# Optimization experiments

Measured on AMD Instinct MI355X. Metric: run time of the kernel, lower is better.

## Reference

```python
import jax, jax.numpy as jnp
import numpy as np

B, CIN, H, W = 2, 3, 768, 768
CB = 32          # backbone out_channels (= channels_mid for heads)
ORDER = 5
MARGIN = 3.0     # ScaledTanh margin of refinement head


def _conv(x, w, b, pad):
    # x: [N,C,H,W], w: [O,I,kh,kw]
    y = jax.lax.conv_general_dilated(x, w, (1, 1), [(pad, pad), (pad, pad)],
                                     dimension_numbers=('NCHW', 'OIHW', 'NCHW'))
    return y + b[None, :, None, None]


def _readout(x, w1, b1, s, t, w2, b2, pad):
    # conv(k) -> batchnorm(eval, folded to scale/shift) -> relu -> dropout(eval=id) -> conv1x1
    h = _conv(x, w1, b1, pad)
    h = jax.nn.relu(h * s[None, :, None, None] + t[None, :, None, None])
    return _conv(h, w2, b2, 0)


def setup_inputs() -> dict:
    key = jax.random.key(0)
    ks = iter(jax.random.split(key, 16))
    def rn(shape, scale=0.05):
        return jax.random.normal(next(ks), shape, jnp.float32) * scale
    d = {'inputs': jax.random.normal(next(ks), (B, CIN, H, W), jnp.float32)}
    d['bb_w'] = rn((CB, CIN, 3, 3)); d['bb_b'] = jnp.zeros((CB,), jnp.float32)
    def head(name, k, cout):
        d[name + '_w1'] = rn((CB, CB, k, k)); d[name + '_b1'] = jnp.zeros((CB,), jnp.float32)
        d[name + '_s'] = jnp.ones((CB,), jnp.float32); d[name + '_t'] = jnp.zeros((CB,), jnp.float32)
        d[name + '_w2'] = rn((cout, CB, 1, 1)); d[name + '_b2'] = jnp.zeros((cout,), jnp.float32)
    head('score', 3, 2)
    head('loc', 7, 2)
    head('four', 7, ORDER * 4)
    head('ref', 7, 2)
    return d


def reference(inputs, bb_w, bb_b,
              score_w1, score_b1, score_s, score_t, score_w2, score_b2,
              loc_w1, loc_b1, loc_s, loc_t, loc_w2, loc_b2,
              four_w1, four_b1, four_s, four_t, four_w2, four_b2,
              ref_w1, ref_b1, ref_s, ref_t, ref_w2, ref_b2):
    # backbone (simple conv + relu; out_channels is an int so contour == refinement features)
    feats = jax.nn.relu(_conv(inputs, bb_w, bb_b, 1))
    scores = _readout(feats, score_w1, score_b1, score_s, score_t, score_w2, score_b2, 1)
    locations = _readout(feats, loc_w1, loc_b1, loc_s, loc_t, loc_w2, loc_b2, 3)
    fourier = _readout(feats, four_w1, four_b1, four_s, four_t, four_w2, four_b2, 3)
    # ReadOut final activation ScaledTanh(3.0), then CPNCore multiplies by internal margin 1.0;
    # feature HW == input HW (stride 1), so F.interpolate is a no-op.
    refinement = jnp.tanh(_readout(feats, ref_w1, ref_b1, ref_s, ref_t, ref_w2, ref_b2, 3)) * MARGIN
    return (scores, locations, refinement, fourier)
```

## Files before the change

kernel.cpp:

```cpp
#include <hip/hip_runtime.h>
#include <hip/hip_bf16.h>
#include <cmath>

#define HH 768
#define WW 768
#define HWSZ (768*768)

typedef __attribute__((ext_vector_type(8))) short bhalf8;
typedef __attribute__((ext_vector_type(4))) float f32x4;
typedef __attribute__((ext_vector_type(16))) float f32x16;

__device__ inline ushort f2bf(float f) {
  __hip_bfloat16 h = __float2bfloat16(f);
  return *reinterpret_cast<ushort*>(&h);
}
__device__ inline float bf2f(ushort u) {
  union { unsigned int i; float f; } v; v.i = ((unsigned int)u) << 16; return v.f;
}

__global__ __launch_bounds__(256) void wxform_all_kernel(
    const float* __restrict__ w1S, const float* __restrict__ b1S,
    const float* __restrict__ sS,  const float* __restrict__ tS,
    const float* __restrict__ w1L, const float* __restrict__ b1L,
    const float* __restrict__ sL,  const float* __restrict__ tL,
    const float* __restrict__ w1F, const float* __restrict__ b1F,
    const float* __restrict__ sF,  const float* __restrict__ tF,
    const float* __restrict__ w1R, const float* __restrict__ b1R,
    const float* __restrict__ sR,  const float* __restrict__ tR,
    ushort* __restrict__ wT0, float* __restrict__ bb0, size_t wt_stride_elems)
{
  int h = blockIdx.y;
  const float *w1, *b1, *s, *t;
  int npos;
  if (h == 0)      { w1 = w1S; b1 = b1S; s = sS; t = tS; npos = 9;  }
  else if (h == 1) { w1 = w1L; b1 = b1L; s = sL; t = tL; npos = 49; }
  else if (h == 2) { w1 = w1F; b1 = b1F; s = sF; t = tF; npos = 49; }
  else             { w1 = w1R; b1 = b1R; s = sR; t = tR; npos = 49; }

  ushort* wT = wT0 + (size_t)h * wt_stride_elems;
  float*  bb = bb0 + h * 32;

  int i = blockIdx.x * 256 + threadIdx.x;
  if (i < npos * 1024) {
    int pos = i >> 10, mc = i & 1023, m = mc >> 5, c = mc & 31;
    wT[i] = f2bf(w1[(m * 32 + c) * npos + pos] * s[m]);
  }
  if (blockIdx.x == 0 && i < 32) bb[i] = b1[i] * s[i] + t[i];
}

__global__ __launch_bounds__(256) void backbone_kernel(
    const float* __restrict__ x, const float* __restrict__ w,
    const float* __restrict__ bias, ushort* __restrict__ feats)
{
  int p = blockIdx.x * 256 + threadIdx.x;
  int bb  = p / HWSZ;
  int rem = p - bb * HWSZ;
  int y   = rem / WW;
  int xx  = rem - y * WW;
  const float* xb = x + (size_t)bb * 3 * HWSZ;

  float v[3][3][3];
  #pragma unroll
  for (int c = 0; c < 3; c++)
    #pragma unroll
    for (int dy = 0; dy < 3; dy++)
      #pragma unroll
      for (int dx = 0; dx < 3; dx++) {
        int yy = y + dy - 1, xq = xx + dx - 1;
        v[c][dy][dx] = (yy >= 0 && yy < HH && xq >= 0 && xq < WW)
                         ? xb[(size_t)c * HWSZ + yy * WW + xq] : 0.f;
      }

  union { ushort u[32]; uint4 q[4]; } pk;
  #pragma unroll
  for (int o = 0; o < 32; o++) {
    float acc = bias[o];
    #pragma unroll
    for (int c = 0; c < 3; c++)
      #pragma unroll
      for (int dy = 0; dy < 3; dy++)
        #pragma unroll
        for (int dx = 0; dx < 3; dx++)
          acc = fmaf(w[((o * 3 + c) * 3 + dy) * 3 + dx], v[c][dy][dx], acc);
    pk.u[o] = f2bf(fmaxf(acc, 0.f));
  }
  uint4* dst = (uint4*)(feats + ((size_t)bb * HWSZ + rem) * 32);
  #pragma unroll
  for (int i = 0; i < 4; i++) dst[i] = pk.q[i];
}

template <int COUT, bool DO_TANH>
__device__ inline void head_epilogue3(
    const f32x16 acc[2], const float* __restrict__ bbh,
    const float* __restrict__ w2, const float* __restrict__ b2,
    float* __restrict__ out_base, ushort* mid,
    int wv, int qr, int qc, int kg, int by, int bx, int bb)
{
  #pragma unroll
  for (int n = 0; n < 2; n++) {
    int px = (2 * wv + qr) * 32 + n * 16 + qc;
    #pragma unroll
    for (int rg = 0; rg < 4; rg++) {
      int m0 = 8 * rg + 4 * kg;
      ushort u[4];
      #pragma unroll
      for (int j = 0; j < 4; j++)
        u[j] = f2bf(fmaxf(acc[n][rg * 4 + j] + bbh[m0 + j], 0.f));
      uint2 pkv;
      pkv.x = (unsigned int)u[0] | ((unsigned int)u[1] << 16);
      pkv.y = (unsigned int)u[2] | ((unsigned int)u[3] << 16);
      *(uint2*)(mid + px * 36 + m0) = pkv;
    }
  }
  __syncthreads();

  int t = threadIdx.x;
  float mv[32];
  #pragma unroll
  for (int j = 0; j < 8; j++) {
    uint2 r = *(const uint2*)(mid + t * 36 + j * 4);
    mv[j * 4 + 0] = bf2f((ushort)(r.x & 0xffff));
    mv[j * 4 + 1] = bf2f((ushort)(r.x >> 16));
    mv[j * 4 + 2] = bf2f((ushort)(r.y & 0xffff));
    mv[j * 4 + 3] = bf2f((ushort)(r.y >> 16));
  }
  int oy = by * 16 + (t >> 5), ox = bx * 32 + (t & 31);
  size_t opix = (size_t)oy * WW + ox;
  float* ob = out_base + (size_t)bb * COUT * HWSZ;
  #pragma unroll
  for (int oc = 0; oc < COUT; oc++) {
    float a2 = b2[oc];
    #pragma unroll
    for (int m = 0; m < 32; m++) a2 = fmaf(w2[oc * 32 + m], mv[m], a2);
    if (DO_TANH) a2 = tanhf(a2) * 3.0f;
    ob[(size_t)oc * HWSZ + opix] = a2;
  }
  __syncthreads();
}

__global__ __launch_bounds__(512, 4) void heads3_kernel(
    const ushort* __restrict__ feats,
    const ushort* __restrict__ wtL, const ushort* __restrict__ wtF,
    const ushort* __restrict__ wtR,
    const float* __restrict__ bbL, const float* __restrict__ bbF,
    const float* __restrict__ bbR,
    const float* __restrict__ w2L, const float* __restrict__ b2L,
    const float* __restrict__ w2F, const float* __restrict__ b2F,
    const float* __restrict__ w2R, const float* __restrict__ b2R,
    float* __restrict__ outL, float* __restrict__ outF, float* __restrict__ outR)
{
  __shared__ __align__(16) char smem[53504 + 24576];
  ushort* tile = (ushort*)smem;
  ushort* wrow = (ushort*)(smem + 53504);

  int bx = blockIdx.x % 24;
  int by = (blockIdx.x / 24) % 48;
  int bb = blockIdx.x / 1152;
  int x0 = bx * 32 - 3, y0 = by * 16 - 3;
  const ushort* fB = feats + (size_t)bb * HWSZ * 32;

  for (int p = threadIdx.x; p < 22 * 38; p += 512) {
    int r = p / 38, cl = p - r * 38;
    int yy = y0 + r, xx = x0 + cl;
    uint4 q0 = {0,0,0,0}, q1 = {0,0,0,0}, q2 = {0,0,0,0}, q3 = {0,0,0,0};
    if (yy >= 0 && yy < HH && xx >= 0 && xx < WW) {
      const uint4* src = (const uint4*)(fB + ((size_t)yy * WW + xx) * 32);
      q0 = src[0]; q1 = src[1]; q2 = src[2]; q3 = src[3];
    }
    ushort* dst = tile + r * 1216 + cl * 8;
    *(uint4*)(dst +   0) = q0;
    *(uint4*)(dst + 304) = q1;
    *(uint4*)(dst + 608) = q2;
    *(uint4*)(dst + 912) = q3;
  }

  int tid = threadIdx.x;
  int l  = tid & 63;
  int wv = tid >> 6;
  int q  = l & 31;
  int kg = l >> 5;
  int qr = q >> 4, qc = q & 15;

  const ushort* pb  = tile + (2 * wv + qr) * 1216 + kg * 304 + qc * 8;
  const ushort* aB  = wrow + kg * 256 + q * 8;
  const ushort* aGL = wtL + q * 32 + kg * 8;
  const ushort* aGF = wtF + q * 32 + kg * 8;
  const ushort* aGR = wtR + q * 32 + kg * 8;

  int st_kx[3], st_src_off[3];
  const ushort* st_base[3];
  #pragma unroll
  for (int j = 0; j < 3; j++) {
    int idx = j * 512 + tid;
    int kx = idx >> 8, rem = idx & 255;
    int h = rem >> 7, g = (rem >> 5) & 3, m = rem & 31;
    st_kx[j] = idx;
    st_base[j] = h ? wtF : wtL;
    st_src_off[j] = kx * 1024 + m * 32 + g * 8;
  }

  f32x16 accL[2] = {};
  f32x16 accF[2] = {};
  f32x16 accR[2] = {};

  #pragma unroll 1
  for (int ky = 0; ky < 7; ky++) {
    __syncthreads();
    #pragma unroll
    for (int j = 0; j < 3; j++) {
      bhalf8 v = *(const bhalf8*)(st_base[j] + ky * 7168 + st_src_off[j]);
      *(bhalf8*)(wrow + st_kx[j] * 8) = v;
    }
    __syncthreads();

    const ushort* pbrow = pb + ky * 1216;
    const ushort* aR = aGR + ky * 7168;

    #pragma unroll
    for (int kx = 0; kx < 7; kx++) {
      bhalf8 fL[2], fF[2], fR[2];
      #pragma unroll
      for (int kh = 0; kh < 2; kh++) {
        if (kx < 6) {
          fL[kh] = *(const bhalf8*)(aB + kx * 2048 +        kh * 512);
          fF[kh] = *(const bhalf8*)(aB + kx * 2048 + 1024 + kh * 512);
        } else {
          fL[kh] = *(const bhalf8*)(aGL + ky * 7168 + 6144 + kh * 16);
          fF[kh] = *(const bhalf8*)(aGF + ky * 7168 + 6144 + kh * 16);
        }
        fR[kh] = *(const bhalf8*)(aR + kx * 1024 + kh * 16);
      }
      bhalf8 bfr[2][2];
      #pragma unroll
      for (int n = 0; n < 2; n++)
        #pragma unroll
        for (int kh = 0; kh < 2; kh++)
          bfr[n][kh] = *(const bhalf8*)(pbrow + kh * 608 + n * 128 + kx * 8);

      #pragma unroll
      for (int n = 0; n < 2; n++)
        #pragma unroll
        for (int kh = 0; kh < 2; kh++) {
          accL[n] = __builtin_amdgcn_mfma_f32_32x32x16_bf16(fL[kh], bfr[n][kh], accL[n], 0, 0, 0);
          accF[n] = __builtin_amdgcn_mfma_f32_32x32x16_bf16(fF[kh], bfr[n][kh], accF[n], 0, 0, 0);
          accR[n] = __builtin_amdgcn_mfma_f32_32x32x16_bf16(fR[kh], bfr[n][kh], accR[n], 0, 0, 0);
        }
    }
  }

  __syncthreads();
  ushort* mid = (ushort*)smem;

  head_epilogue3<2,  false>(accL, bbL, w2L, b2L, outL, mid, wv, qr, qc, kg, by, bx, bb);
  head_epilogue3<20, false>(accF, bbF, w2F, b2F, outF, mid, wv, qr, qc, kg, by, bx, bb);
  head_epilogue3<2,  true >(accR, bbR, w2R, b2R, outR, mid, wv, qr, qc, kg, by, bx, bb);
}

typedef __attribute__((ext_vector_type(4))) float f32x4b;
template <int COUT, bool DO_TANH>
__device__ inline void head_epilogue_s(
    const f32x16 acc[2], const float* __restrict__ bbh,
    const float* __restrict__ w2, const float* __restrict__ b2,
    float* __restrict__ out_base, float* mid,
    int wv, int qr, int qc, int kg, int by, int bx, int bb)
{
  #pragma unroll
  for (int n = 0; n < 2; n++) {
    int pix = (wv * 4 + 2 * n + qr) * 16 + qc;
    #pragma unroll
    for (int rg = 0; rg < 4; rg++) {
      int m0 = 8 * rg + 4 * kg;
      f32x4 v;
      #pragma unroll
      for (int j = 0; j < 4; j++)
        v[j] = fmaxf(acc[n][rg * 4 + j] + bbh[m0 + j], 0.f);
      *(f32x4*)(mid + pix * 36 + m0) = v;
    }
  }
  __syncthreads();

  int t = threadIdx.x;
  float mv[32];
  #pragma unroll
  for (int j2 = 0; j2 < 8; j2++)
    *(f32x4*)(mv + 4 * j2) = *(const f32x4*)(mid + t * 36 + 4 * j2);

  int oy = by * 16 + (t >> 4), ox = bx * 16 + (t & 15);
  size_t opix = (size_t)oy * WW + ox;
  float* ob = out_base + (size_t)bb * COUT * HWSZ;
  #pragma unroll
  for (int oc = 0; oc < COUT; oc++) {
    float a2 = b2[oc];
    #pragma unroll
    for (int m = 0; m < 32; m++) a2 = fmaf(w2[oc * 32 + m], mv[m], a2);
    if (DO_TANH) a2 = tanhf(a2) * 3.0f;
    ob[(size_t)oc * HWSZ + opix] = a2;
  }
}

__global__ __launch_bounds__(256, 4) void score_kernel(
    const ushort* __restrict__ feats,
    const ushort* __restrict__ wtS, const float* __restrict__ bbS,
    const float* __restrict__ w2S, const float* __restrict__ b2S,
    float* __restrict__ outS)
{
  constexpr int TW = 18, CPAD = 40;
  constexpr int SMEM_BYTES = 256 * 36 * 4;
  __shared__ __align__(16) char smem[SMEM_BYTES];
  ushort* tile = (ushort*)smem;

  int bx = blockIdx.x % 48;
  int by = (blockIdx.x / 48) % 48;
  int bb = blockIdx.x / 2304;
  int x0 = bx * 16 - 1, y0 = by * 16 - 1;
  const ushort* fB = feats + (size_t)bb * HWSZ * 32;

  for (int p = threadIdx.x; p < TW * TW; p += 256) {
    int py = p / TW, pxx = p % TW;
    int yy = y0 + py, xx = x0 + pxx;
    uint4 q0 = {0,0,0,0}, q1 = {0,0,0,0}, q2 = {0,0,0,0}, q3 = {0,0,0,0};
    if (yy >= 0 && yy < HH && xx >= 0 && xx < WW) {
      const uint4* src = (const uint4*)(fB + ((size_t)yy * WW + xx) * 32);
      q0 = src[0]; q1 = src[1]; q2 = src[2]; q3 = src[3];
    }
    uint4* dst = (uint4*)(tile + (size_t)p * CPAD);
    dst[0] = q0; dst[1] = q1; dst[2] = q2; dst[3] = q3;
  }
  __syncthreads();

  int l  = threadIdx.x & 63;
  int wv = threadIdx.x >> 6;
  int q  = l & 31;
  int kg = l >> 5;
  int qr = q >> 4, qc = q & 15;

  const ushort* pb = tile + ((wv * 4 + qr) * TW + qc) * CPAD + kg * 8;
  const int aoff = q * 32 + kg * 8;

  f32x16 acc[2] = {};

  #pragma unroll
  for (int ky = 0; ky < 3; ky++) {
    #pragma unroll
    for (int kx = 0; kx < 3; kx++) {
      const int tap = ky * 3 + kx;
      bhalf8 a0[2];
      #pragma unroll
      for (int kh = 0; kh < 2; kh++)
        a0[kh] = *(const bhalf8*)(wtS + tap * 1024 + aoff + kh * 16);
      #pragma unroll
      for (int n = 0; n < 2; n++) {
        #pragma unroll
        for (int kh = 0; kh < 2; kh++) {
          bhalf8 bf = *(const bhalf8*)(pb + (ky * TW + kx) * CPAD
                                          + n * 2 * TW * CPAD + kh * 16);
          acc[n] = __builtin_amdgcn_mfma_f32_32x32x16_bf16(a0[kh], bf, acc[n], 0, 0, 0);
        }
      }
    }
  }

  __syncthreads();
  float* mid = (float*)smem;
  head_epilogue_s<2, false>(acc, bbS, w2S, b2S, outS, mid, wv, qr, qc, kg, by, bx, bb);
}

extern "C" void kernel_launch(void* const* d_in, const int* in_sizes, int n_in,
                              void* d_out, int out_size, void* d_ws, size_t ws_size,
                              hipStream_t stream) {
  const float* input = (const float*)d_in[0];
  const float* bb_w  = (const float*)d_in[1];
  const float* bb_b  = (const float*)d_in[2];

  ushort* feats = (ushort*)d_ws;
  char* base = (char*)d_ws;
  const size_t FEATS_BYTES = (size_t)2 * HWSZ * 32 * 2;
  const size_t WT_STRIDE_E = 49 * 1024;
  ushort* wT0 = (ushort*)(base + FEATS_BYTES);
  float*  bb0 = (float*)(base + FEATS_BYTES + 4 * WT_STRIDE_E * 2);
  (void)out_size; (void)ws_size; (void)n_in; (void)in_sizes;

  float* out = (float*)d_out;
  float* outS = out;
  float* outL = out + (size_t)4  * HWSZ;
  float* outR = out + (size_t)8  * HWSZ;
  float* outF = out + (size_t)12 * HWSZ;

  dim3 wxgrid(196, 4);
  wxform_all_kernel<<<wxgrid, 256, 0, stream>>>(
      (const float*)d_in[3],  (const float*)d_in[4],  (const float*)d_in[5],  (const float*)d_in[6],
      (const float*)d_in[9],  (const float*)d_in[10], (const float*)d_in[11], (const float*)d_in[12],
      (const float*)d_in[15], (const float*)d_in[16], (const float*)d_in[17], (const float*)d_in[18],
      (const float*)d_in[21], (const float*)d_in[22], (const float*)d_in[23], (const float*)d_in[24],
      wT0, bb0, WT_STRIDE_E);

  backbone_kernel<<<4608, 256, 0, stream>>>(input, bb_w, bb_b, feats);

  const ushort* wtS = wT0 + 0 * WT_STRIDE_E;
  const ushort* wtL = wT0 + 1 * WT_STRIDE_E;
  const ushort* wtF = wT0 + 2 * WT_STRIDE_E;
  const ushort* wtR = wT0 + 3 * WT_STRIDE_E;

  heads3_kernel<<<2 * 48 * 24, 512, 0, stream>>>(
      feats, wtL, wtF, wtR,
      bb0 + 32, bb0 + 64, bb0 + 96,
      (const float*)d_in[13], (const float*)d_in[14],
      (const float*)d_in[19], (const float*)d_in[20],
      (const float*)d_in[25], (const float*)d_in[26],
      outL, outF, outR);

  score_kernel<<<2 * 48 * 48, 256, 0, stream>>>(
      feats, wtS, bb0 + 0,
      (const float*)d_in[7], (const float*)d_in[8], outS);
}
```

Baseline: 435.1 us.

## Prefetch next weight row into registers and raise MFMA wave priority

```diff
diff --git a/kernel.cpp b/kernel.cpp
--- a/kernel.cpp
+++ b/kernel.cpp
@@ -138,7 +138,7 @@
   __syncthreads();
 }
 
-__global__ __launch_bounds__(512, 4) void heads3_kernel(
+__global__ __launch_bounds__(512, 2) void heads3_kernel(
     const ushort* __restrict__ feats,
     const ushort* __restrict__ wtL, const ushort* __restrict__ wtF,
     const ushort* __restrict__ wtR,
@@ -187,17 +187,24 @@
   const ushort* aGF = wtF + q * 32 + kg * 8;
   const ushort* aGR = wtR + q * 32 + kg * 8;
 
-  int st_kx[3], st_src_off[3];
-  const ushort* st_base[3];
-  #pragma unroll
-  for (int j = 0; j < 3; j++) {
-    int idx = j * 512 + tid;
-    int kx = idx >> 8, rem = idx & 255;
-    int h = rem >> 7, g = (rem >> 5) & 3, m = rem & 31;
-    st_kx[j] = idx;
-    st_base[j] = h ? wtF : wtL;
-    st_src_off[j] = kx * 1024 + m * 32 + g * 8;
-  }
+  const ushort* stp0; const ushort* stp1; const ushort* stp2;
+  {
+    int idx, kx, rem, h, g, m;
+    idx = tid;        kx = idx >> 8; rem = idx & 255; h = rem >> 7; g = (rem >> 5) & 3; m = rem & 31;
+    stp0 = (h ? wtF : wtL) + kx * 1024 + m * 32 + g * 8;
+    idx = 512 + tid;  kx = idx >> 8; rem = idx & 255; h = rem >> 7; g = (rem >> 5) & 3; m = rem & 31;
+    stp1 = (h ? wtF : wtL) + kx * 1024 + m * 32 + g * 8;
+    idx = 1024 + tid; kx = idx >> 8; rem = idx & 255; h = rem >> 7; g = (rem >> 5) & 3; m = rem & 31;
+    stp2 = (h ? wtF : wtL) + kx * 1024 + m * 32 + g * 8;
+  }
+  ushort* std0 = wrow + (size_t)tid * 8;
+  ushort* std1 = wrow + (size_t)(512 + tid) * 8;
+  ushort* std2 = wrow + (size_t)(1024 + tid) * 8;
+
+  bhalf8 pA0 = *(const bhalf8*)(stp0);
+  bhalf8 pA1 = *(const bhalf8*)(stp1);
+  bhalf8 pA2 = *(const bhalf8*)(stp2);
+  bhalf8 pB0 = pA0, pB1 = pA1, pB2 = pA2;
 
   f32x16 accL[2] = {};
   f32x16 accF[2] = {};
@@ -206,12 +213,16 @@
   #pragma unroll 1
   for (int ky = 0; ky < 7; ky++) {
     __syncthreads();
-    #pragma unroll
-    for (int j = 0; j < 3; j++) {
-      bhalf8 v = *(const bhalf8*)(st_base[j] + ky * 7168 + st_src_off[j]);
-      *(bhalf8*)(wrow + st_kx[j] * 8) = v;
-    }
+    *(bhalf8*)std0 = pA0;
+    *(bhalf8*)std1 = pA1;
+    *(bhalf8*)std2 = pA2;
     __syncthreads();
+
+    if (ky < 6) {
+      pB0 = *(const bhalf8*)(stp0 + (ky + 1) * 7168);
+      pB1 = *(const bhalf8*)(stp1 + (ky + 1) * 7168);
+      pB2 = *(const bhalf8*)(stp2 + (ky + 1) * 7168);
+    }
 
     const ushort* pbrow = pb + ky * 1216;
     const ushort* aR = aGR + ky * 7168;
@@ -237,6 +248,7 @@
         for (int kh = 0; kh < 2; kh++)
           bfr[n][kh] = *(const bhalf8*)(pbrow + kh * 608 + n * 128 + kx * 8);
 
+      __builtin_amdgcn_s_setprio(1);
       #pragma unroll
       for (int n = 0; n < 2; n++)
         #pragma unroll
@@ -245,7 +257,10 @@
           accF[n] = __builtin_amdgcn_mfma_f32_32x32x16_bf16(fF[kh], bfr[n][kh], accF[n], 0, 0, 0);
           accR[n] = __builtin_amdgcn_mfma_f32_32x32x16_bf16(fR[kh], bfr[n][kh], accR[n], 0, 0, 0);
         }
-    }
+      __builtin_amdgcn_s_setprio(0);
+    }
+
+    pA0 = pB0; pA1 = pB1; pA2 = pB2;
   }
 
   __syncthreads();
@@ -256,7 +271,6 @@
   head_epilogue3<2,  true >(accR, bbR, w2R, b2R, outR, mid, wv, qr, qc, kg, by, bx, bb);
 }
 
-typedef __attribute__((ext_vector_type(4))) float f32x4b;
 template <int COUT, bool DO_TANH>
 __device__ inline void head_epilogue_s(
     const f32x16 acc[2], const float* __restrict__ bbh,
```

Measured after the change: 427.9 us. About the same (-1.6%).

## Load head weights directly from global with register prefetch, drop LDS weight staging

Applied to the files above, without the earlier changes.

```diff
diff --git a/kernel.cpp b/kernel.cpp
--- a/kernel.cpp
+++ b/kernel.cpp
@@ -138,7 +138,7 @@
   __syncthreads();
 }
 
-__global__ __launch_bounds__(512, 4) void heads3_kernel(
+__global__ __launch_bounds__(512, 2) void heads3_kernel(
     const ushort* __restrict__ feats,
     const ushort* __restrict__ wtL, const ushort* __restrict__ wtF,
     const ushort* __restrict__ wtR,
@@ -149,9 +149,8 @@
     const float* __restrict__ w2R, const float* __restrict__ b2R,
     float* __restrict__ outL, float* __restrict__ outF, float* __restrict__ outR)
 {
-  __shared__ __align__(16) char smem[53504 + 24576];
+  __shared__ __align__(16) char smem[53504];
   ushort* tile = (ushort*)smem;
-  ushort* wrow = (ushort*)(smem + 53504);
 
   int bx = blockIdx.x % 24;
   int by = (blockIdx.x / 24) % 48;
@@ -173,6 +172,7 @@
     *(uint4*)(dst + 608) = q2;
     *(uint4*)(dst + 912) = q3;
   }
+  __syncthreads();
 
   int tid = threadIdx.x;
   int l  = tid & 63;
@@ -182,69 +182,77 @@
   int qr = q >> 4, qc = q & 15;
 
   const ushort* pb  = tile + (2 * wv + qr) * 1216 + kg * 304 + qc * 8;
-  const ushort* aB  = wrow + kg * 256 + q * 8;
   const ushort* aGL = wtL + q * 32 + kg * 8;
   const ushort* aGF = wtF + q * 32 + kg * 8;
   const ushort* aGR = wtR + q * 32 + kg * 8;
 
-  int st_kx[3], st_src_off[3];
-  const ushort* st_base[3];
-  #pragma unroll
-  for (int j = 0; j < 3; j++) {
-    int idx = j * 512 + tid;
-    int kx = idx >> 8, rem = idx & 255;
-    int h = rem >> 7, g = (rem >> 5) & 3, m = rem & 31;
-    st_kx[j] = idx;
-    st_base[j] = h ? wtF : wtL;
-    st_src_off[j] = kx * 1024 + m * 32 + g * 8;
-  }
-
   f32x16 accL[2] = {};
   f32x16 accF[2] = {};
   f32x16 accR[2] = {};
 
   #pragma unroll 1
   for (int ky = 0; ky < 7; ky++) {
-    __syncthreads();
-    #pragma unroll
-    for (int j = 0; j < 3; j++) {
-      bhalf8 v = *(const bhalf8*)(st_base[j] + ky * 7168 + st_src_off[j]);
-      *(bhalf8*)(wrow + st_kx[j] * 8) = v;
-    }
-    __syncthreads();
-
+    const ushort* aL = aGL + ky * 7168;
+    const ushort* aF = aGF + ky * 7168;
+    const ushort* aR = aGR + ky * 7168;
     const ushort* pbrow = pb + ky * 1216;
-    const ushort* aR = aGR + ky * 7168;
+
+    bhalf8 fL[7][2], fF[7][2], fR[7][2];
+    #pragma unroll
+    for (int kx = 0; kx < 2; kx++) {
+      fL[kx][0] = *(const bhalf8*)(aL + kx * 1024);
+      fL[kx][1] = *(const bhalf8*)(aL + kx * 1024 + 16);
+      fF[kx][0] = *(const bhalf8*)(aF + kx * 1024);
+      fF[kx][1] = *(const bhalf8*)(aF + kx * 1024 + 16);
+      fR[kx][0] = *(const bhalf8*)(aR + kx * 1024);
+      fR[kx][1] = *(const bhalf8*)(aR + kx * 1024 + 16);
+    }
+
+    bhalf8 cB00 = *(const bhalf8*)(pbrow);
+    bhalf8 cB01 = *(const bhalf8*)(pbrow + 608);
+    bhalf8 cB10 = *(const bhalf8*)(pbrow + 128);
+    bhalf8 cB11 = *(const bhalf8*)(pbrow + 608 + 128);
 
     #pragma unroll
     for (int kx = 0; kx < 7; kx++) {
-      bhalf8 fL[2], fF[2], fR[2];
-      #pragma unroll
-      for (int kh = 0; kh < 2; kh++) {
-        if (kx < 6) {
-          fL[kh] = *(const bhalf8*)(aB + kx * 2048 +        kh * 512);
-          fF[kh] = *(const bhalf8*)(aB + kx * 2048 + 1024 + kh * 512);
-        } else {
-          fL[kh] = *(const bhalf8*)(aGL + ky * 7168 + 6144 + kh * 16);
-          fF[kh] = *(const bhalf8*)(aGF + ky * 7168 + 6144 + kh * 16);
-        }
-        fR[kh] = *(const bhalf8*)(aR + kx * 1024 + kh * 16);
+      if (kx + 2 < 7) {
+        const ushort* a2L = aL + (kx + 2) * 1024;
+        const ushort* a2F = aF + (kx + 2) * 1024;
+        const ushort* a2R = aR + (kx + 2) * 1024;
+        fL[kx + 2][0] = *(const bhalf8*)(a2L);
+        fL[kx + 2][1] = *(const bhalf8*)(a2L + 16);
+        fF[kx + 2][0] = *(const bhalf8*)(a2F);
+        fF[kx + 2][1] = *(const bhalf8*)(a2F + 16);
+        fR[kx + 2][0] = *(const bhalf8*)(a2R);
+        fR[kx + 2][1] = *(const bhalf8*)(a2R + 16);
       }
-      bhalf8 bfr[2][2];
-      #pragma unroll
-      for (int n = 0; n < 2; n++)
-        #pragma unroll
-        for (int kh = 0; kh < 2; kh++)
-          bfr[n][kh] = *(const bhalf8*)(pbrow + kh * 608 + n * 128 + kx * 8);
-
-      #pragma unroll
-      for (int n = 0; n < 2; n++)
-        #pragma unroll
-        for (int kh = 0; kh < 2; kh++) {
-          accL[n] = __builtin_amdgcn_mfma_f32_32x32x16_bf16(fL[kh], bfr[n][kh], accL[n], 0, 0, 0);
-          accF[n] = __builtin_amdgcn_mfma_f32_32x32x16_bf16(fF[kh], bfr[n][kh], accF[n], 0, 0, 0);
-          accR[n] = __builtin_amdgcn_mfma_f32_32x32x16_bf16(fR[kh], bfr[n][kh], accR[n], 0, 0, 0);
-        }
+      bhalf8 nB00, nB01, nB10, nB11;
+      if (kx < 6) {
+        const ushort* p2 = pbrow + (kx + 1) * 8;
+        nB00 = *(const bhalf8*)(p2);
+        nB01 = *(const bhalf8*)(p2 + 608);
+        nB10 = *(const bhalf8*)(p2 + 128);
+        nB11 = *(const bhalf8*)(p2 + 608 + 128);
+      }
+
+      __builtin_amdgcn_s_setprio(1);
+      accL[0] = __builtin_amdgcn_mfma_f32_32x32x16_bf16(fL[kx][0], cB00, accL[0], 0, 0, 0);
+      accL[0] = __builtin_amdgcn_mfma_f32_32x32x16_bf16(fL[kx][1], cB01, accL[0], 0, 0, 0);
+      accL[1] = __builtin_amdgcn_mfma_f32_32x32x16_bf16(fL[kx][0], cB10, accL[1], 0, 0, 0);
+      accL[1] = __builtin_amdgcn_mfma_f32_32x32x16_bf16(fL[kx][1], cB11, accL[1], 0, 0, 0);
+      accF[0] = __builtin_amdgcn_mfma_f32_32x32x16_bf16(fF[kx][0], cB00, accF[0], 0, 0, 0);
+      accF[0] = __builtin_amdgcn_mfma_f32_32x32x16_bf16(fF[kx][1], cB01, accF[0], 0, 0, 0);
+      accF[1] = __builtin_amdgcn_mfma_f32_32x32x16_bf16(fF[kx][0], cB10, accF[1], 0, 0, 0);
+      accF[1] = __builtin_amdgcn_mfma_f32_32x32x16_bf16(fF[kx][1], cB11, accF[1], 0, 0, 0);
+      accR[0] = __builtin_amdgcn_mfma_f32_32x32x16_bf16(fR[kx][0], cB00, accR[0], 0, 0, 0);
+      accR[0] = __builtin_amdgcn_mfma_f32_32x32x16_bf16(fR[kx][1], cB01, accR[0], 0, 0, 0);
+      accR[1] = __builtin_amdgcn_mfma_f32_32x32x16_bf16(fR[kx][0], cB10, accR[1], 0, 0, 0);
+      accR[1] = __builtin_amdgcn_mfma_f32_32x32x16_bf16(fR[kx][1], cB11, accR[1], 0, 0, 0);
+      __builtin_amdgcn_s_setprio(0);
+
+      if (kx < 6) {
+        cB00 = nB00; cB01 = nB01; cB10 = nB10; cB11 = nB11;
+      }
     }
   }
 
@@ -256,7 +264,6 @@
   head_epilogue3<2,  true >(accR, bbR, w2R, b2R, outR, mid, wv, qr, qc, kg, by, bx, bb);
 }
 
-typedef __attribute__((ext_vector_type(4))) float f32x4b;
 template <int COUT, bool DO_TANH>
 __device__ inline void head_epilogue_s(
     const f32x16 acc[2], const float* __restrict__ bbh,
```

After: 481.5 us. +10.7%, slower.
